# Optimization experiments

Measured on AMD Instinct MI355X. Metric: run time of the kernel, lower is better.

## Reference

```python
import jax, jax.numpy as jnp
import numpy as np

N_NODES = 50000
N_EDGES = 800000
D_IN = 512
D_OUT = 512


def sage_conv(x, src, dst, Wl, Wr, b, num_nodes):
    # PyG SAGEConv (mean aggr): out = lin_l(mean_{j in N(i)} x_j) + lin_r(x_i) + bias
    msg = x[src]                                            # [E, d]
    summed = jax.ops.segment_sum(msg, dst, num_segments=num_nodes)  # [N, d]
    cnt = jax.ops.segment_sum(jnp.ones((src.shape[0],), dtype=x.dtype), dst,
                              num_segments=num_nodes)        # [N]
    mean = summed / jnp.maximum(cnt, 1.0)[:, None]           # isolated nodes -> 0
    return mean @ Wl.T + x @ Wr.T + b


def setup_inputs() -> dict:
    key = jax.random.key(0)
    ks = jax.random.split(key, 8)
    s = 1.0 / np.sqrt(D_IN)
    x = jax.random.normal(ks[0], (N_NODES, D_IN), dtype=jnp.float32)
    edge_index = jax.random.randint(ks[1], (2, N_EDGES), 0, N_NODES, dtype=jnp.int64)
    Wl1 = jax.random.normal(ks[2], (D_OUT, D_IN), dtype=jnp.float32) * s
    Wr1 = jax.random.normal(ks[3], (D_OUT, D_IN), dtype=jnp.float32) * s
    b1 = jnp.zeros((D_OUT,), dtype=jnp.float32)
    Wl2 = jax.random.normal(ks[4], (D_IN, D_OUT), dtype=jnp.float32) * s
    Wr2 = jax.random.normal(ks[5], (D_IN, D_OUT), dtype=jnp.float32) * s
    b2 = jnp.zeros((D_IN,), dtype=jnp.float32)
    return {"x": x, "edge_index": edge_index, "Wl1": Wl1, "Wr1": Wr1, "b1": b1,
            "Wl2": Wl2, "Wr2": Wr2, "b2": b2}


def reference(x, edge_index, Wl1, Wr1, b1, Wl2, Wr2, b2):
    src, dst = edge_index[0], edge_index[1]
    n = x.shape[0]
    h = sage_conv(x, src, dst, Wl1, Wr1, b1, n)
    h = jax.nn.relu(h)
    return sage_conv(h, src, dst, Wl2, Wr2, b2, n)
```

## Files before the change

kernel.cpp:

```cpp
#include <hip/hip_runtime.h>
#include <hip/hip_fp8.h>

typedef __bf16 bf16_t;
typedef __bf16 bf16x8 __attribute__((ext_vector_type(8)));
typedef __bf16 bf16x4 __attribute__((ext_vector_type(4)));
typedef float  f32x4  __attribute__((ext_vector_type(4)));
typedef float  f32x2  __attribute__((ext_vector_type(2)));

#define D_FEAT 512
#define M_TILES 392
#define NPAD2 (M_TILES * 128)
#define N_TILES 4
#define GEMM_BLOCKS (M_TILES * N_TILES)
#define XBLOCKS (NPAD2 / 4)

__device__ __forceinline__ float fp8_to_f32(unsigned int b) {
  __hip_fp8_e4m3 q;
  q.__x = (__hip_fp8_storage_t)b;
  return (float)q;
}
__device__ __forceinline__ unsigned char f32_to_fp8(float v) {
  __hip_fp8_e4m3 q(v);
  return (unsigned char)q.__x;
}

__global__ void cvt_all_k(const float* __restrict__ x, bf16_t* __restrict__ xb,
                          unsigned char* __restrict__ x8, int valid,
                          const float* __restrict__ Wl1, const float* __restrict__ Wr1,
                          bf16_t* __restrict__ WB1,
                          const float* __restrict__ Wl2, const float* __restrict__ Wr2,
                          bf16_t* __restrict__ WB2,
                          const int* __restrict__ dst, int* __restrict__ deg, int E) {
  int b = blockIdx.x;
  bf16x8 o;
  if (b < XBLOCKS) {
    int idx = (b * 256 + threadIdx.x) * 8;
    float e[8];
    if (idx < valid) {
      const float4* p = (const float4*)(x + idx);
      float4 a = p[0], c = p[1];
      e[0] = a.x; e[1] = a.y; e[2] = a.z; e[3] = a.w;
      e[4] = c.x; e[5] = c.y; e[6] = c.z; e[7] = c.w;
    } else {
#pragma unroll
      for (int i = 0; i < 8; ++i) e[i] = 0.f;
    }
#pragma unroll
    for (int i = 0; i < 8; ++i) o[i] = (bf16_t)e[i];
    *(bf16x8*)(xb + idx) = o;
    if (x8) {
      unsigned int lo = 0, hi = 0;
#pragma unroll
      for (int i = 0; i < 4; ++i) lo |= (unsigned int)f32_to_fp8(e[i]) << (8 * i);
#pragma unroll
      for (int i = 0; i < 4; ++i) hi |= (unsigned int)f32_to_fp8(e[4 + i]) << (8 * i);
      uint2 pk; pk.x = lo; pk.y = hi;
      *(uint2*)(x8 + idx) = pk;
    }
  } else if (b < XBLOCKS + 512) {
    int wb = b - XBLOCKS;
    const float* Wl = (wb < 256) ? Wl1 : Wl2;
    const float* Wr = (wb < 256) ? Wr1 : Wr2;
    bf16_t* WB = (wb < 256) ? WB1 : WB2;
    int idx = ((wb & 255) * 256 + threadIdx.x) * 8;
    int n = idx >> 10, k = idx & 1023;
    const float* s = (k < 512) ? (Wl + n * 512 + k) : (Wr + n * 512 + k - 512);
    const float4* p = (const float4*)s;
    float4 a = p[0], c = p[1];
    o[0] = (bf16_t)a.x; o[1] = (bf16_t)a.y; o[2] = (bf16_t)a.z; o[3] = (bf16_t)a.w;
    o[4] = (bf16_t)c.x; o[5] = (bf16_t)c.y; o[6] = (bf16_t)c.z; o[7] = (bf16_t)c.w;
    *(bf16x8*)(WB + idx) = o;
  } else {
    int e = (b - XBLOCKS - 512) * 256 + threadIdx.x;
    if (e < E) atomicAdd(&deg[dst[e]], 1);
  }
}

__global__ void scan_part_k(const int* __restrict__ deg, int* __restrict__ partial, int N) {
  __shared__ int sd[512];
  int tid = threadIdx.x;
  int i = blockIdx.x * 512 + tid;
  sd[tid] = (i < N) ? deg[i] : 0;
  __syncthreads();
  for (int s = 256; s > 0; s >>= 1) {
    if (tid < s) sd[tid] += sd[tid + s];
    __syncthreads();
  }
  if (tid == 0) partial[blockIdx.x] = sd[0];
}

__global__ void scan_off_k(int* __restrict__ partial, int nb, int* __restrict__ rowS, int N) {
  __shared__ int sd[128];
  int tid = threadIdx.x;
  int v = (tid < nb) ? partial[tid] : 0;
  sd[tid] = v;
  __syncthreads();
#pragma unroll
  for (int offd = 1; offd < 128; offd <<= 1) {
    int t = (tid >= offd) ? sd[tid - offd] : 0;
    __syncthreads();
    sd[tid] += t;
    __syncthreads();
  }
  if (tid < nb) partial[tid] = sd[tid] - v;
  if (tid == nb - 1) rowS[N] = sd[tid];
}

__global__ void scan_blk_k(const int* __restrict__ deg, const int* __restrict__ partial,
                           int* __restrict__ rowS, int* __restrict__ cursor, int N) {
  __shared__ int sd[512];
  int tid = threadIdx.x;
  int i = blockIdx.x * 512 + tid;
  int v = (i < N) ? deg[i] : 0;
  sd[tid] = v;
  __syncthreads();
  for (int offd = 1; offd < 512; offd <<= 1) {
    int t = (tid >= offd) ? sd[tid - offd] : 0;
    __syncthreads();
    sd[tid] += t;
    __syncthreads();
  }
  int excl = sd[tid] - v + partial[blockIdx.x];
  if (i < N) { rowS[i] = excl; cursor[i] = excl; }
}

__global__ void scat_k(const int* __restrict__ src, const int* __restrict__ dst,
                       int* __restrict__ cursor, int* __restrict__ col, int E) {
  int e = blockIdx.x * 256 + threadIdx.x;
  if (e < E) {
    int d = dst[e];
    int p = atomicAdd(&cursor[d], 1);
    col[p] = src[e];
  }
}

template <bool FP8>
__global__ __launch_bounds__(256) void agg_k(const void* __restrict__ Xv,
                                             const int* __restrict__ rs,
                                             const int* __restrict__ col,
                                             bf16_t* __restrict__ out,
                                             int N) {
  const int lane = threadIdx.x & 63;
  const int node = blockIdx.x * 4 + (threadIdx.x >> 6);
  const size_t obase = (size_t)node * D_FEAT + lane * 8;
  bf16x8 o;
  if (node >= N) {
#pragma unroll
    for (int i = 0; i < 8; ++i) o[i] = (bf16_t)0.f;
    *(bf16x8*)(out + obase) = o;
    return;
  }
  const int s = rs[node], e = rs[node + 1];
  float acc[8] = {0.f, 0.f, 0.f, 0.f, 0.f, 0.f, 0.f, 0.f};
  int j = s;
  if (FP8) {
    const unsigned char* X8 = (const unsigned char*)Xv;
    const int loff = lane * 8;
    auto addv = [&](uint2 v) {
#if __has_builtin(__builtin_amdgcn_cvt_pk_f32_fp8)
      f32x2 p0 = __builtin_amdgcn_cvt_pk_f32_fp8((int)v.x, false);
      f32x2 p1 = __builtin_amdgcn_cvt_pk_f32_fp8((int)v.x, true);
      f32x2 p2 = __builtin_amdgcn_cvt_pk_f32_fp8((int)v.y, false);
      f32x2 p3 = __builtin_amdgcn_cvt_pk_f32_fp8((int)v.y, true);
      acc[0] += p0[0]; acc[1] += p0[1]; acc[2] += p1[0]; acc[3] += p1[1];
      acc[4] += p2[0]; acc[5] += p2[1]; acc[6] += p3[0]; acc[7] += p3[1];
#else
#pragma unroll
      for (int i = 0; i < 4; ++i) acc[i] += fp8_to_f32((v.x >> (8 * i)) & 0xff);
#pragma unroll
      for (int i = 0; i < 4; ++i) acc[4 + i] += fp8_to_f32((v.y >> (8 * i)) & 0xff);
#endif
    };
    for (; j + 8 <= e; j += 8) {
      int c0 = col[j + 0], c1 = col[j + 1], c2 = col[j + 2], c3 = col[j + 3];
      int c4 = col[j + 4], c5 = col[j + 5], c6 = col[j + 6], c7 = col[j + 7];
      uint2 v0 = *(const uint2*)(X8 + (size_t)c0 * D_FEAT + loff);
      uint2 v1 = *(const uint2*)(X8 + (size_t)c1 * D_FEAT + loff);
      uint2 v2 = *(const uint2*)(X8 + (size_t)c2 * D_FEAT + loff);
      uint2 v3 = *(const uint2*)(X8 + (size_t)c3 * D_FEAT + loff);
      uint2 v4 = *(const uint2*)(X8 + (size_t)c4 * D_FEAT + loff);
      uint2 v5 = *(const uint2*)(X8 + (size_t)c5 * D_FEAT + loff);
      uint2 v6 = *(const uint2*)(X8 + (size_t)c6 * D_FEAT + loff);
      uint2 v7 = *(const uint2*)(X8 + (size_t)c7 * D_FEAT + loff);
      addv(v0); addv(v1); addv(v2); addv(v3);
      addv(v4); addv(v5); addv(v6); addv(v7);
    }
    for (; j < e; ++j) {
      uint2 v = *(const uint2*)(X8 + (size_t)col[j] * D_FEAT + loff);
      addv(v);
    }
  } else {
    const bf16_t* X = (const bf16_t*)Xv;
    const int loff = lane * 8;
    for (; j + 8 <= e; j += 8) {
      int c0 = col[j + 0], c1 = col[j + 1], c2 = col[j + 2], c3 = col[j + 3];
      int c4 = col[j + 4], c5 = col[j + 5], c6 = col[j + 6], c7 = col[j + 7];
      bf16x8 v0 = *(const bf16x8*)(X + (size_t)c0 * D_FEAT + loff);
      bf16x8 v1 = *(const bf16x8*)(X + (size_t)c1 * D_FEAT + loff);
      bf16x8 v2 = *(const bf16x8*)(X + (size_t)c2 * D_FEAT + loff);
      bf16x8 v3 = *(const bf16x8*)(X + (size_t)c3 * D_FEAT + loff);
      bf16x8 v4 = *(const bf16x8*)(X + (size_t)c4 * D_FEAT + loff);
      bf16x8 v5 = *(const bf16x8*)(X + (size_t)c5 * D_FEAT + loff);
      bf16x8 v6 = *(const bf16x8*)(X + (size_t)c6 * D_FEAT + loff);
      bf16x8 v7 = *(const bf16x8*)(X + (size_t)c7 * D_FEAT + loff);
#pragma unroll
      for (int i = 0; i < 8; ++i) {
        float s01 = (float)v0[i] + (float)v1[i];
        float s23 = (float)v2[i] + (float)v3[i];
        float s45 = (float)v4[i] + (float)v5[i];
        float s67 = (float)v6[i] + (float)v7[i];
        acc[i] += (s01 + s23) + (s45 + s67);
      }
    }
    for (; j < e; ++j) {
      bf16x8 v0 = *(const bf16x8*)(X + (size_t)col[j] * D_FEAT + loff);
#pragma unroll
      for (int i = 0; i < 8; ++i) acc[i] += (float)v0[i];
    }
  }
  float sc = (e > s) ? 1.0f / (float)(e - s) : 0.f;
#pragma unroll
  for (int i = 0; i < 8; ++i) o[i] = (bf16_t)(acc[i] * sc);
  *(bf16x8*)(out + obase) = o;
}

__device__ __forceinline__ void gload_lds16(const void* g, void* l) {
  __builtin_amdgcn_global_load_lds(
      (const __attribute__((address_space(1))) unsigned int*)g,
      (__attribute__((address_space(3))) unsigned int*)l,
      16, 0, 0);
}

template <bool RELU, bool HAS8, typename OT>
__global__ __launch_bounds__(256, 2) void gemm_k(
    const bf16_t* __restrict__ A0,
    const bf16_t* __restrict__ A1,
    const bf16_t* __restrict__ WB,
    const float* __restrict__ bias,
    OT* __restrict__ out,
    unsigned char* __restrict__ out8,
    int M) {
  const int t = (blockIdx.x & 7) * (GEMM_BLOCKS / 8) + (blockIdx.x >> 3);
  const int mt = t >> 2;
  const int nt = t & 3;

  __shared__ __align__(16) unsigned short smem[2 * 16384];

  const int tid = threadIdx.x;
  const int lane = tid & 63;
  const int wave = tid >> 6;
  const int wr = wave >> 1;
  const int wc = wave & 1;
  const int m0 = mt * 128;
  const int n0 = nt * 128;

  f32x4 acc[4][4];
#pragma unroll
  for (int m = 0; m < 4; ++m)
#pragma unroll
    for (int n = 0; n < 4; ++n) acc[m][n] = (f32x4){0.f, 0.f, 0.f, 0.f};

  const int srow = tid >> 3;
  const int sslot = tid & 7;
  const int kc = sslot ^ (srow & 7);
  const int ldsOff = srow * 64 + sslot * 8;
  size_t gA[4], gB[4];
#pragma unroll
  for (int l = 0; l < 4; ++l) {
    gA[l] = (size_t)(m0 + l * 32 + srow) * 1024 + kc * 16;
    gB[l] = (size_t)(n0 + l * 32 + srow) * 2048 + kc * 16;
  }

  auto stage = [&](int buf, int kk) {
    unsigned short* sA = smem + buf * 16384;
    unsigned short* sB = sA + 8192;
    const int k0 = kk * 64;
    const char* Ab = (k0 < 512) ? (const char*)A0 : (const char*)A1;
    const size_t ka = (size_t)(k0 & 511) * 2;
    const size_t kb = (size_t)k0 * 2;
#pragma unroll
    for (int l = 0; l < 4; ++l) {
      gload_lds16(Ab + gA[l] + ka, sA + ldsOff + l * 2048);
      gload_lds16((const char*)WB + gB[l] + kb, sB + ldsOff + l * 2048);
    }
  };

  const int fr = lane & 15;
  const int g = lane >> 4;
  int rdA[2][4], rdB[2][4];
#pragma unroll
  for (int ks = 0; ks < 2; ++ks) {
    const int sl = ((ks * 4 + g) ^ (fr & 7)) * 8;
#pragma unroll
    for (int m = 0; m < 4; ++m) rdA[ks][m] = (wr * 64 + m * 16 + fr) * 64 + sl;
#pragma unroll
    for (int n = 0; n < 4; ++n) rdB[ks][n] = (wc * 64 + n * 16 + fr) * 64 + sl;
  }

  stage(0, 0);
  stage(1, 1);
  __builtin_amdgcn_sched_barrier(0);

  const int NK = 16;
  for (int kk = 0; kk < NK; ++kk) {
    const int cur = kk & 1;
    if (kk < NK - 1) {
      asm volatile("s_waitcnt vmcnt(8)" ::: "memory");
    } else {
      asm volatile("s_waitcnt vmcnt(0)" ::: "memory");
    }
    __builtin_amdgcn_sched_barrier(0);
    __builtin_amdgcn_s_barrier();
    __builtin_amdgcn_sched_barrier(0);

    unsigned short* sA = smem + cur * 16384;
    unsigned short* sB = sA + 8192;
    __builtin_amdgcn_s_setprio(1);
#pragma unroll
    for (int ks = 0; ks < 2; ++ks) {
      bf16x8 aF[4], bF[4];
#pragma unroll
      for (int m = 0; m < 4; ++m) aF[m] = *(const bf16x8*)(sA + rdA[ks][m]);
#pragma unroll
      for (int n = 0; n < 4; ++n) bF[n] = *(const bf16x8*)(sB + rdB[ks][n]);
#pragma unroll
      for (int m = 0; m < 4; ++m)
#pragma unroll
        for (int n = 0; n < 4; ++n)
          acc[m][n] = __builtin_amdgcn_mfma_f32_16x16x32_bf16(aF[m], bF[n], acc[m][n], 0, 0, 0);
    }
    __builtin_amdgcn_s_setprio(0);

    __builtin_amdgcn_sched_barrier(0);
    __builtin_amdgcn_s_barrier();
    __builtin_amdgcn_sched_barrier(0);
    if (kk + 2 < NK) stage(cur, kk + 2);
    __builtin_amdgcn_sched_barrier(0);
  }

  float bv[4];
#pragma unroll
  for (int n = 0; n < 4; ++n) bv[n] = bias[n0 + wc * 64 + n * 16 + fr];

  OT* sE = (OT*)smem;
#pragma unroll
  for (int h = 0; h < 2; ++h) {
    __syncthreads();
    if (wc == h) {
#pragma unroll
      for (int n = 0; n < 4; ++n) {
        const int colL = n * 16 + fr;
#pragma unroll
        for (int m = 0; m < 4; ++m) {
          const int rbase = wr * 64 + m * 16 + g * 4;
#pragma unroll
          for (int r = 0; r < 4; ++r) {
            float v = acc[m][n][r] + bv[n];
            if (RELU) v = fmaxf(v, 0.f);
            sE[(rbase + r) * 68 + colL] = (OT)v;
          }
        }
      }
    }
    __syncthreads();
    const int rL0 = tid >> 4;
    const int colL = (tid & 15) * 4;
    const int gcol = n0 + h * 64 + colL;
#pragma unroll
    for (int p = 0; p < 8; ++p) {
      const int rowL = p * 16 + rL0;
      const int grow = m0 + rowL;
      if (grow < M) {
        if constexpr (sizeof(OT) == 4) {
          f32x4 v = *(const f32x4*)&sE[rowL * 68 + colL];
          *(f32x4*)((float*)out + (size_t)grow * 512 + gcol) = v;
        } else {
          bf16x4 v = *(const bf16x4*)&sE[rowL * 68 + colL];
          *(bf16x4*)((bf16_t*)out + (size_t)grow * 512 + gcol) = v;
          if (HAS8) {
            unsigned int u = 0;
#pragma unroll
            for (int i = 0; i < 4; ++i)
              u |= (unsigned int)f32_to_fp8((float)v[i]) << (8 * i);
            *(unsigned int*)(out8 + (size_t)grow * 512 + gcol) = u;
          }
        }
      }
    }
  }
}

extern "C" void kernel_launch(void* const* d_in, const int* in_sizes, int n_in,
                              void* d_out, int out_size, void* d_ws, size_t ws_size,
                              hipStream_t stream) {
  const float* x   = (const float*)d_in[0];
  const int*   ei  = (const int*)d_in[1];
  const float* Wl1 = (const float*)d_in[2];
  const float* Wr1 = (const float*)d_in[3];
  const float* b1  = (const float*)d_in[4];
  const float* Wl2 = (const float*)d_in[5];
  const float* Wr2 = (const float*)d_in[6];
  const float* b2  = (const float*)d_in[7];

  const int N = in_sizes[0] / 512;
  const int E = in_sizes[1] / 2;
  const int* srcp = ei;
  const int* dstp = ei + E;

  char* ws = (char*)d_ws;
  size_t off = 0;
  auto alloc = [&](size_t sz) -> char* {
    char* p = ws + off;
    off += sz;
    off = (off + 255) & ~(size_t)255;
    return p;
  };

  bf16_t* xb    = (bf16_t*)alloc((size_t)NPAD2 * 512 * 2);
  bf16_t* hb    = (bf16_t*)alloc((size_t)NPAD2 * 512 * 2);
  bf16_t* meanb = (bf16_t*)alloc((size_t)NPAD2 * 512 * 2);
  bf16_t* WB1   = (bf16_t*)alloc((size_t)512 * 1024 * 2);
  bf16_t* WB2   = (bf16_t*)alloc((size_t)512 * 1024 * 2);
  int* deg      = (int*)alloc((size_t)N * 4);
  int* rowS     = (int*)alloc((size_t)(N + 8) * 4);
  int* cursor   = (int*)alloc((size_t)N * 4);
  int* partial  = (int*)alloc(4096);
  int* colb     = (int*)alloc((size_t)E * 4);
  unsigned char* x8 = (unsigned char*)alloc((size_t)NPAD2 * 512);
  unsigned char* h8 = (unsigned char*)alloc((size_t)NPAD2 * 512);
  const bool useFp8 = (off <= ws_size);
  (void)n_in; (void)out_size;

  hipMemsetAsync(deg, 0, (size_t)N * 4, stream);

  const int degBlocks = (E + 255) / 256;
  cvt_all_k<<<dim3(XBLOCKS + 512 + degBlocks), dim3(256), 0, stream>>>(
      x, xb, useFp8 ? x8 : nullptr, N * 512, Wl1, Wr1, WB1, Wl2, Wr2, WB2,
      dstp, deg, E);

  int NB = (N + 511) / 512;
  scan_part_k<<<dim3(NB), dim3(512), 0, stream>>>(deg, partial, N);
  scan_off_k<<<dim3(1), dim3(128), 0, stream>>>(partial, NB, rowS, N);
  scan_blk_k<<<dim3(NB), dim3(512), 0, stream>>>(deg, partial, rowS, cursor, N);
  scat_k<<<dim3((E + 255) / 256), dim3(256), 0, stream>>>(srcp, dstp, cursor, colb, E);

  dim3 agrid(NPAD2 / 4);
  dim3 grid(GEMM_BLOCKS);

  if (useFp8) {
    agg_k<true><<<agrid, dim3(256), 0, stream>>>(x8, rowS, colb, meanb, N);
    gemm_k<true, true, bf16_t><<<grid, dim3(256), 0, stream>>>(meanb, xb, WB1, b1, hb, h8, NPAD2);
    agg_k<true><<<agrid, dim3(256), 0, stream>>>(h8, rowS, colb, meanb, N);
    gemm_k<false, false, float><<<grid, dim3(256), 0, stream>>>(meanb, hb, WB2, b2, (float*)d_out, nullptr, N);
  } else {
    agg_k<false><<<agrid, dim3(256), 0, stream>>>(xb, rowS, colb, meanb, N);
    gemm_k<true, false, bf16_t><<<grid, dim3(256), 0, stream>>>(meanb, xb, WB1, b1, hb, nullptr, NPAD2);
    agg_k<false><<<agrid, dim3(256), 0, stream>>>(hb, rowS, colb, meanb, N);
    gemm_k<false, false, float><<<grid, dim3(256), 0, stream>>>(meanb, hb, WB2, b2, (float*)d_out, nullptr, N);
  }
}
```

Baseline: 393.9 us.

## Enlarge GEMM tile to 256x128 with 8 waves and fuse scan kernels

The GEMM tile grows from 128x128 to 256x128 and runs with 512 threads (8 waves), while the K step shrinks from 64 to 32 with a new 4-slot XOR swizzle. Each tile of weights B is then reused across more rows and fewer blocks are launched. The single-block offset scan is folded into the per-block scan: every block redundantly rescans the partial sums, which removes one kernel launch. The cost is more LDS per block (about 68KB), a shallower K step per barrier, and NPAD2 padding that stays at the same total size. The epilogue staging buffer must now hold 256 rows; for float output at stride 68 that needs about 69.6KB, which the 69888-byte allocation covers.

```diff
diff --git a/kernel.cpp b/kernel.cpp
--- a/kernel.cpp
+++ b/kernel.cpp
@@ -8,8 +8,8 @@
 typedef float  f32x2  __attribute__((ext_vector_type(2)));
 
 #define D_FEAT 512
-#define M_TILES 392
-#define NPAD2 (M_TILES * 128)
+#define M_TILES 196
+#define NPAD2 (M_TILES * 256)
 #define N_TILES 4
 #define GEMM_BLOCKS (M_TILES * N_TILES)
 #define XBLOCKS (NPAD2 / 4)
@@ -89,27 +89,21 @@
   if (tid == 0) partial[blockIdx.x] = sd[0];
 }
 
-__global__ void scan_off_k(int* __restrict__ partial, int nb, int* __restrict__ rowS, int N) {
-  __shared__ int sd[128];
-  int tid = threadIdx.x;
-  int v = (tid < nb) ? partial[tid] : 0;
-  sd[tid] = v;
-  __syncthreads();
-#pragma unroll
-  for (int offd = 1; offd < 128; offd <<= 1) {
-    int t = (tid >= offd) ? sd[tid - offd] : 0;
-    __syncthreads();
-    sd[tid] += t;
-    __syncthreads();
-  }
-  if (tid < nb) partial[tid] = sd[tid] - v;
-  if (tid == nb - 1) rowS[N] = sd[tid];
-}
-
-__global__ void scan_blk_k(const int* __restrict__ deg, const int* __restrict__ partial,
-                           int* __restrict__ rowS, int* __restrict__ cursor, int N) {
+__global__ void scan_blk2_k(const int* __restrict__ deg, const int* __restrict__ partial,
+                            int* __restrict__ rowS, int* __restrict__ cursor, int N, int nb) {
+  __shared__ int sp[128];
   __shared__ int sd[512];
   int tid = threadIdx.x;
+  if (tid < 128) sp[tid] = (tid < nb) ? partial[tid] : 0;
+  __syncthreads();
+#pragma unroll
+  for (int off = 1; off < 128; off <<= 1) {
+    int t = (tid >= off && tid < 128) ? sp[tid - off] : 0;
+    __syncthreads();
+    if (tid < 128) sp[tid] += t;
+    __syncthreads();
+  }
+  const int blkoff = sp[blockIdx.x] - partial[blockIdx.x];
   int i = blockIdx.x * 512 + tid;
   int v = (i < N) ? deg[i] : 0;
   sd[tid] = v;
@@ -120,8 +114,9 @@
     sd[tid] += t;
     __syncthreads();
   }
-  int excl = sd[tid] - v + partial[blockIdx.x];
+  int excl = sd[tid] - v + blkoff;
   if (i < N) { rowS[i] = excl; cursor[i] = excl; }
+  if (blockIdx.x == 0 && tid == 0) rowS[N] = sp[nb - 1];
 }
 
 __global__ void scat_k(const int* __restrict__ src, const int* __restrict__ dst,
@@ -232,7 +227,7 @@
 }
 
 template <bool RELU, bool HAS8, typename OT>
-__global__ __launch_bounds__(256, 2) void gemm_k(
+__global__ __launch_bounds__(512, 4) void gemm_k(
     const bf16_t* __restrict__ A0,
     const bf16_t* __restrict__ A1,
     const bf16_t* __restrict__ WB,
@@ -244,14 +239,15 @@
   const int mt = t >> 2;
   const int nt = t & 3;
 
-  __shared__ __align__(16) unsigned short smem[2 * 16384];
+  __shared__ __align__(16) unsigned char smemraw[69888];
+  unsigned short* smem = (unsigned short*)smemraw;
 
   const int tid = threadIdx.x;
   const int lane = tid & 63;
   const int wave = tid >> 6;
-  const int wr = wave >> 1;
-  const int wc = wave & 1;
-  const int m0 = mt * 128;
+  const int wm = wave >> 1;
+  const int wn = wave & 1;
+  const int m0 = mt * 256;
   const int n0 = nt * 128;
 
   f32x4 acc[4][4];
@@ -260,52 +256,46 @@
 #pragma unroll
     for (int n = 0; n < 4; ++n) acc[m][n] = (f32x4){0.f, 0.f, 0.f, 0.f};
 
-  const int srow = tid >> 3;
-  const int sslot = tid & 7;
-  const int kc = sslot ^ (srow & 7);
-  const int ldsOff = srow * 64 + sslot * 8;
-  size_t gA[4], gB[4];
-#pragma unroll
-  for (int l = 0; l < 4; ++l) {
-    gA[l] = (size_t)(m0 + l * 32 + srow) * 1024 + kc * 16;
-    gB[l] = (size_t)(n0 + l * 32 + srow) * 2048 + kc * 16;
-  }
+  const int srow = tid >> 2;
+  const int sslot = tid & 3;
+  const int kc = sslot ^ ((srow >> 1) & 3);
+  const int ldsOffA = srow * 32 + sslot * 8;
+  size_t gA[2], gB;
+#pragma unroll
+  for (int l = 0; l < 2; ++l)
+    gA[l] = (size_t)(m0 + l * 128 + srow) * 1024 + kc * 16;
+  gB = (size_t)(n0 + srow) * 2048 + kc * 16;
 
   auto stage = [&](int buf, int kk) {
-    unsigned short* sA = smem + buf * 16384;
+    unsigned short* sA = smem + buf * 12288;
     unsigned short* sB = sA + 8192;
-    const int k0 = kk * 64;
+    const int k0 = kk * 32;
     const char* Ab = (k0 < 512) ? (const char*)A0 : (const char*)A1;
     const size_t ka = (size_t)(k0 & 511) * 2;
     const size_t kb = (size_t)k0 * 2;
-#pragma unroll
-    for (int l = 0; l < 4; ++l) {
-      gload_lds16(Ab + gA[l] + ka, sA + ldsOff + l * 2048);
-      gload_lds16((const char*)WB + gB[l] + kb, sB + ldsOff + l * 2048);
-    }
+    gload_lds16(Ab + gA[0] + ka, sA + ldsOffA);
+    gload_lds16(Ab + gA[1] + ka, sA + 4096 + ldsOffA);
+    gload_lds16((const char*)WB + gB + kb, sB + ldsOffA);
   };
 
   const int fr = lane & 15;
   const int g = lane >> 4;
-  int rdA[2][4], rdB[2][4];
-#pragma unroll
-  for (int ks = 0; ks < 2; ++ks) {
-    const int sl = ((ks * 4 + g) ^ (fr & 7)) * 8;
-#pragma unroll
-    for (int m = 0; m < 4; ++m) rdA[ks][m] = (wr * 64 + m * 16 + fr) * 64 + sl;
-#pragma unroll
-    for (int n = 0; n < 4; ++n) rdB[ks][n] = (wc * 64 + n * 16 + fr) * 64 + sl;
-  }
+  const int sl = (g ^ ((fr >> 1) & 3)) * 8;
+  int rdA[4], rdB[4];
+#pragma unroll
+  for (int m = 0; m < 4; ++m) rdA[m] = (wm * 64 + m * 16 + fr) * 32 + sl;
+#pragma unroll
+  for (int n = 0; n < 4; ++n) rdB[n] = (wn * 64 + n * 16 + fr) * 32 + sl;
 
   stage(0, 0);
   stage(1, 1);
   __builtin_amdgcn_sched_barrier(0);
 
-  const int NK = 16;
+  const int NK = 32;
   for (int kk = 0; kk < NK; ++kk) {
     const int cur = kk & 1;
     if (kk < NK - 1) {
-      asm volatile("s_waitcnt vmcnt(8)" ::: "memory");
+      asm volatile("s_waitcnt vmcnt(3)" ::: "memory");
     } else {
       asm volatile("s_waitcnt vmcnt(0)" ::: "memory");
     }
@@ -313,22 +303,19 @@
     __builtin_amdgcn_s_barrier();
     __builtin_amdgcn_sched_barrier(0);
 
-    unsigned short* sA = smem + cur * 16384;
+    unsigned short* sA = smem + cur * 12288;
     unsigned short* sB = sA + 8192;
+    bf16x8 aF[4], bF[4];
     __builtin_amdgcn_s_setprio(1);
 #pragma unroll
-    for (int ks = 0; ks < 2; ++ks) {
-      bf16x8 aF[4], bF[4];
-#pragma unroll
-      for (int m = 0; m < 4; ++m) aF[m] = *(const bf16x8*)(sA + rdA[ks][m]);
-#pragma unroll
-      for (int n = 0; n < 4; ++n) bF[n] = *(const bf16x8*)(sB + rdB[ks][n]);
-#pragma unroll
-      for (int m = 0; m < 4; ++m)
-#pragma unroll
-        for (int n = 0; n < 4; ++n)
-          acc[m][n] = __builtin_amdgcn_mfma_f32_16x16x32_bf16(aF[m], bF[n], acc[m][n], 0, 0, 0);
-    }
+    for (int m = 0; m < 4; ++m) aF[m] = *(const bf16x8*)(sA + rdA[m]);
+#pragma unroll
+    for (int n = 0; n < 4; ++n) bF[n] = *(const bf16x8*)(sB + rdB[n]);
+#pragma unroll
+    for (int m = 0; m < 4; ++m)
+#pragma unroll
+      for (int n = 0; n < 4; ++n)
+        acc[m][n] = __builtin_amdgcn_mfma_f32_16x16x32_bf16(aF[m], bF[n], acc[m][n], 0, 0, 0);
     __builtin_amdgcn_s_setprio(0);
 
     __builtin_amdgcn_sched_barrier(0);
@@ -340,19 +327,19 @@
 
   float bv[4];
 #pragma unroll
-  for (int n = 0; n < 4; ++n) bv[n] = bias[n0 + wc * 64 + n * 16 + fr];
-
-  OT* sE = (OT*)smem;
+  for (int n = 0; n < 4; ++n) bv[n] = bias[n0 + wn * 64 + n * 16 + fr];
+
+  OT* sE = (OT*)smemraw;
 #pragma unroll
   for (int h = 0; h < 2; ++h) {
     __syncthreads();
-    if (wc == h) {
+    if (wn == h) {
 #pragma unroll
       for (int n = 0; n < 4; ++n) {
         const int colL = n * 16 + fr;
 #pragma unroll
         for (int m = 0; m < 4; ++m) {
-          const int rbase = wr * 64 + m * 16 + g * 4;
+          const int rbase = wm * 64 + m * 16 + g * 4;
 #pragma unroll
           for (int r = 0; r < 4; ++r) {
             float v = acc[m][n][r] + bv[n];
@@ -368,7 +355,7 @@
     const int gcol = n0 + h * 64 + colL;
 #pragma unroll
     for (int p = 0; p < 8; ++p) {
-      const int rowL = p * 16 + rL0;
+      const int rowL = p * 32 + rL0;
       const int grow = m0 + rowL;
       if (grow < M) {
         if constexpr (sizeof(OT) == 4) {
@@ -440,8 +427,7 @@
 
   int NB = (N + 511) / 512;
   scan_part_k<<<dim3(NB), dim3(512), 0, stream>>>(deg, partial, N);
-  scan_off_k<<<dim3(1), dim3(128), 0, stream>>>(partial, NB, rowS, N);
-  scan_blk_k<<<dim3(NB), dim3(512), 0, stream>>>(deg, partial, rowS, cursor, N);
+  scan_blk2_k<<<dim3(NB), dim3(512), 0, stream>>>(deg, partial, rowS, cursor, N, NB);
   scat_k<<<dim3((E + 255) / 256), dim3(256), 0, stream>>>(srcp, dstp, cursor, colb, E);
 
   dim3 agrid(NPAD2 / 4);
@@ -449,13 +435,13 @@
 
   if (useFp8) {
     agg_k<true><<<agrid, dim3(256), 0, stream>>>(x8, rowS, colb, meanb, N);
-    gemm_k<true, true, bf16_t><<<grid, dim3(256), 0, stream>>>(meanb, xb, WB1, b1, hb, h8, NPAD2);
+    gemm_k<true, true, bf16_t><<<grid, dim3(512), 0, stream>>>(meanb, xb, WB1, b1, hb, h8, NPAD2);
     agg_k<true><<<agrid, dim3(256), 0, stream>>>(h8, rowS, colb, meanb, N);
-    gemm_k<false, false, float><<<grid, dim3(256), 0, stream>>>(meanb, hb, WB2, b2, (float*)d_out, nullptr, N);
+    gemm_k<false, false, float><<<grid, dim3(512), 0, stream>>>(meanb, hb, WB2, b2, (float*)d_out, nullptr, N);
   } else {
     agg_k<false><<<agrid, dim3(256), 0, stream>>>(xb, rowS, colb, meanb, N);
-    gemm_k<true, false, bf16_t><<<grid, dim3(256), 0, stream>>>(meanb, xb, WB1, b1, hb, nullptr, NPAD2);
+    gemm_k<true, false, bf16_t><<<grid, dim3(512), 0, stream>>>(meanb, xb, WB1, b1, hb, nullptr, NPAD2);
     agg_k<false><<<agrid, dim3(256), 0, stream>>>(hb, rowS, colb, meanb, N);
-    gemm_k<false, false, float><<<grid, dim3(256), 0, stream>>>(meanb, hb, WB2, b2, (float*)d_out, nullptr, N);
-  }
-}
+    gemm_k<false, false, float><<<grid, dim3(512), 0, stream>>>(meanb, hb, WB2, b2, (float*)d_out, nullptr, N);
+  }
+}
```

New measurement: 397.9 us. About the same (+1.0%).
